# Kernel tuning notes

Hardware: AMD Instinct MI355X
Metric: run time of the kernel (lower is better)

## Reference

```python
import jax, jax.numpy as jnp
import numpy as np

C = 128  # n_atom_basis


def setup_inputs() -> dict:
    key = jax.random.key(0)
    k_h, k_A, k_Ww, k_Wb, k_aw, k_ab = jax.random.split(key, 6)
    B, N = 8, 2048
    h = jax.random.normal(k_h, (B, N, C), dtype=jnp.float32)
    A = jax.random.uniform(k_A, (B, N, N), dtype=jnp.float32)
    # nn.Linear(C, C)
    lim_W = 1.0 / np.sqrt(C)
    W_w = jax.random.uniform(k_Ww, (C, C), minval=-lim_W, maxval=lim_W, dtype=jnp.float32)
    W_b = jax.random.uniform(k_Wb, (C,), minval=-lim_W, maxval=lim_W, dtype=jnp.float32)
    # nn.Linear(2C, 1)
    lim_a = 1.0 / np.sqrt(2 * C)
    a_w = jax.random.uniform(k_aw, (2 * C,), minval=-lim_a, maxval=lim_a, dtype=jnp.float32)
    a_b = jax.random.uniform(k_ab, (), minval=-lim_a, maxval=lim_a, dtype=jnp.float32)
    return {"h": h, "A": A, "W_w": W_w, "W_b": W_b, "a_w": a_w, "a_b": a_b}


def reference(h, A, W_w, W_b, a_w, a_b):
    # Wh computed once ([B,N,C]) instead of the original's redundant [B,N,N,C] broadcast.
    Wh = jnp.einsum('bnc,dc->bnd', h, W_w) + W_b
    # a([hi, hj]) = a_w[:C]@Wh_i + a_w[C:]@Wh_j + a_b  -> rank-1 decomposition of the concat-linear
    si = Wh @ a_w[:C]          # [B,N]
    sj = Wh @ a_w[C:]          # [B,N]
    s = si[:, :, None] + sj[:, None, :] + a_b  # [B,N,N] raw scores
    e = jnp.exp(s) * A                          # masked exp (no max-subtraction: matches original math)
    alpha = e / jnp.sum(e, axis=2, keepdims=True)
    # weighted sum over neighbors j of the ORIGINAL h (as in the source, not Wh)
    h_prime = jnp.einsum('bij,bjc->bic', alpha, h)
    return h_prime
```

## Files before the change

### kernel.cpp

```cpp
#include <hip/hip_runtime.h>
#include <math.h>
#include <stdint.h>

#define Bn 8
#define Nn 2048
#define Cn 128
#define CP 144
#define NKB (Nn / 32)

typedef _Float16 f16x8 __attribute__((ext_vector_type(8)));
typedef _Float16 f16x2 __attribute__((ext_vector_type(2)));
typedef __fp16   fp16x2 __attribute__((ext_vector_type(2)));
typedef float    f32x4 __attribute__((ext_vector_type(4)));

__device__ __forceinline__ void dma16(const void* g, void* l) {
    __builtin_amdgcn_global_load_lds((const __attribute__((address_space(1))) uint32_t*)g,
                                     (__attribute__((address_space(3))) uint32_t*)l,
                                     16, 0, 0);
}

__global__ __launch_bounds__(256) void rows_kernel(const float* __restrict__ h,
                                                   const float* __restrict__ Ww,
                                                   const float* __restrict__ Wb,
                                                   const float* __restrict__ aw,
                                                   _Float16* __restrict__ hWt) {
    __shared__ float tile[16][132];
    __shared__ float vlo[128];
    __shared__ float vhi[128];
    __shared__ float wsh[16];
    __shared__ float b2sh;

    int bid = blockIdx.x;
    int b   = bid & 7;
    int n0  = (bid >> 3) << 4;
    int tid = threadIdx.x;

    {
        int c = tid & 127, half = tid >> 7;
        float acc = 0.f;
#pragma unroll
        for (int dd = 0; dd < 64; ++dd) {
            int d = half * 64 + dd;
            acc += Ww[d * Cn + c] * aw[Cn + d];
        }
        if (half) vhi[c] = acc; else vlo[c] = acc;
    }
    if (tid < 64) {
        float b2p = Wb[tid] * aw[Cn + tid] + Wb[tid + 64] * aw[Cn + tid + 64];
        b2p += __shfl_xor(b2p, 32, 64);
        b2p += __shfl_xor(b2p, 16, 64);
        b2p += __shfl_xor(b2p, 8, 64);
        b2p += __shfl_xor(b2p, 4, 64);
        b2p += __shfl_xor(b2p, 2, 64);
        b2p += __shfl_xor(b2p, 1, 64);
        if (tid == 0) b2sh = b2p;
    }
    {
#pragma unroll
        for (int i = 0; i < 2; ++i) {
            int idx = tid + 256 * i;
            int r = idx >> 5, f4 = idx & 31;
            *(float4*)&tile[r][f4 * 4] =
                ((const float4*)(h + (size_t)(b * Nn + n0 + r) * Cn))[f4];
        }
    }
    __syncthreads();

    {
        int r = tid >> 4, g = tid & 15;
        float acc = 0.f;
#pragma unroll
        for (int ii = 0; ii < 8; ++ii) {
            int i = g * 8 + ii;
            acc += tile[r][i] * (vlo[i] + vhi[i]);
        }
        acc += __shfl_xor(acc, 1, 64);
        acc += __shfl_xor(acc, 2, 64);
        acc += __shfl_xor(acc, 4, 64);
        acc += __shfl_xor(acc, 8, 64);
        if (g == 0) wsh[r] = expf(acc + b2sh);
    }
    __syncthreads();

    {
        int kb = n0 >> 5, khalf = (n0 >> 4) & 1;
        _Float16* hWb = hWt + ((size_t)(b * NKB + kb) * CP) * 32 + khalf * 16;
#pragma unroll
        for (int i = 0; i < 5; ++i) {
            int idx = tid + 256 * i;
            if (idx < 1152) {
                int cp = idx >> 3, p = idx & 7;
                int r0 = p * 2;
                f16x2 v2;
                if (cp < 128) {
                    v2[0] = (_Float16)(wsh[r0] * tile[r0][cp]);
                    v2[1] = (_Float16)(wsh[r0 + 1] * tile[r0 + 1][cp]);
                } else if (cp == 128) {
                    v2[0] = (_Float16)wsh[r0];
                    v2[1] = (_Float16)wsh[r0 + 1];
                } else {
                    v2[0] = (_Float16)0.f;
                    v2[1] = (_Float16)0.f;
                }
                *(f16x2*)(hWb + (size_t)cp * 32 + p * 2) = v2;
            }
        }
    }
}

__global__ __launch_bounds__(256, 4) void attn_kernel(const float* __restrict__ A,
                                                      const _Float16* __restrict__ hWt,
                                                      float* __restrict__ out) {
    __shared__ float Alds[2][16 * 64];
    __shared__ float den[16];

    int bid = blockIdx.x;
    int b   = bid & 7;
    int i0  = (bid >> 3) << 4;
    int koff = ((bid >> 3) * 5 + (bid & 7)) & 31;
    int tid = threadIdx.x;
    int wv  = tid >> 6, l = tid & 63;
    int m   = l & 15, q = l >> 4;

    const float*    Ab  = A   + (size_t)(b * Nn + i0) * Nn;
    const _Float16* hWb = hWt + (size_t)b * NKB * CP * 32;

    int sr  = wv * 4 + q;
    int skq = (m - sr) & 15;
    const float* sg = Ab + (size_t)sr * Nn + skq * 4;
    float* sl = &Alds[0][0] + wv * 256;

    f32x4 acc[3];
#pragma unroll
    for (int s = 0; s < 3; ++s) acc[s] = (f32x4){0.f, 0.f, 0.f, 0.f};

    dma16(sg + (size_t)koff * 64, sl);

    for (int t = 0; t < 32; ++t) {
        int buf = t & 1;
        __syncthreads();
        if (t < 31)
            dma16(sg + (size_t)((t + 1 + koff) & 31) * 64,
                  sl + (buf ^ 1) * (16 * 64));

        int kb = (t + koff) & 31;
        f16x8 bf[6];
#pragma unroll
        for (int ksub = 0; ksub < 2; ++ksub)
#pragma unroll
            for (int s = 0; s < 3; ++s) {
                int ct = (s == 2) ? 8 : wv * 2 + s;
                bf[ksub * 3 + s] = *(const f16x8*)(
                    hWb + ((size_t)(kb * 2 + ksub) * CP + ct * 16 + m) * 32 + q * 8);
            }
#pragma unroll
        for (int ksub = 0; ksub < 2; ++ksub) {
            int kq0 = ksub * 8 + 2 * q;
            float4 x = *(const float4*)&Alds[buf][m * 64 + ((kq0 + m) & 15) * 4];
            float4 y = *(const float4*)&Alds[buf][m * 64 + ((kq0 + 1 + m) & 15) * 4];
            union { fp16x2 h2[4]; f16x8 v; } u;
            u.h2[0] = __builtin_amdgcn_cvt_pkrtz(x.x, x.y);
            u.h2[1] = __builtin_amdgcn_cvt_pkrtz(x.z, x.w);
            u.h2[2] = __builtin_amdgcn_cvt_pkrtz(y.x, y.y);
            u.h2[3] = __builtin_amdgcn_cvt_pkrtz(y.z, y.w);
#pragma unroll
            for (int s = 0; s < 3; ++s)
                acc[s] = __builtin_amdgcn_mfma_f32_16x16x32_f16(u.v, bf[ksub * 3 + s],
                                                                acc[s], 0, 0, 0);
        }
    }

    if (wv == 0 && m == 0) {
#pragma unroll
        for (int r = 0; r < 4; ++r) den[q * 4 + r] = acc[2][r];
    }
    __syncthreads();

#pragma unroll
    for (int r = 0; r < 4; ++r) {
        float invd = 1.f / den[q * 4 + r];
        float* ob = out + (size_t)(b * Nn + i0 + q * 4 + r) * Cn;
#pragma unroll
        for (int s = 0; s < 2; ++s)
            ob[(wv * 2 + s) * 16 + m] = acc[s][r] * invd;
    }
}

extern "C" void kernel_launch(void* const* d_in, const int* in_sizes, int n_in,
                              void* d_out, int out_size, void* d_ws, size_t ws_size,
                              hipStream_t stream) {
    const float* h  = (const float*)d_in[0];
    const float* A  = (const float*)d_in[1];
    const float* Ww = (const float*)d_in[2];
    const float* Wb = (const float*)d_in[3];
    const float* aw = (const float*)d_in[4];
    float* out = (float*)d_out;

    _Float16* hWt = (_Float16*)d_ws;

    rows_kernel<<<Bn * (Nn / 16), 256, 0, stream>>>(h, Ww, Wb, aw, hWt);
    attn_kernel<<<Bn * (Nn / 16), 256, 0, stream>>>(A, hWt, out);
}
```

Baseline: 242.9 us.

## Enlarge attention tile to 32 rows with register-staged fp16 A in LDS

The attention kernel now processes 32 query rows per block with 512 threads. Each wave owns one 16-column output tile across two row tiles, so each hW B-fragment load is reused twice. A is loaded into registers, converted to fp16 once, and stored in LDS. This replaces the async global-to-LDS DMA of fp32 and the per-wave reconversion. The change is meant to halve B-operand traffic per output and cut conversion work, at the cost of a synchronous register-staged prefetch pipeline and the loss of the staggered k-offset.

```diff
diff --git a/kernel.cpp b/kernel.cpp
--- a/kernel.cpp
+++ b/kernel.cpp
@@ -9,15 +9,10 @@
 #define NKB (Nn / 32)
 
 typedef _Float16 f16x8 __attribute__((ext_vector_type(8)));
+typedef _Float16 f16x4 __attribute__((ext_vector_type(4)));
 typedef _Float16 f16x2 __attribute__((ext_vector_type(2)));
 typedef __fp16   fp16x2 __attribute__((ext_vector_type(2)));
 typedef float    f32x4 __attribute__((ext_vector_type(4)));
-
-__device__ __forceinline__ void dma16(const void* g, void* l) {
-    __builtin_amdgcn_global_load_lds((const __attribute__((address_space(1))) uint32_t*)g,
-                                     (__attribute__((address_space(3))) uint32_t*)l,
-                                     16, 0, 0);
-}
 
 __global__ __launch_bounds__(256) void rows_kernel(const float* __restrict__ h,
                                                    const float* __restrict__ Ww,
@@ -108,16 +103,15 @@
     }
 }
 
-__global__ __launch_bounds__(256, 4) void attn_kernel(const float* __restrict__ A,
+__global__ __launch_bounds__(512, 4) void attn_kernel(const float* __restrict__ A,
                                                       const _Float16* __restrict__ hWt,
                                                       float* __restrict__ out) {
-    __shared__ float Alds[2][16 * 64];
-    __shared__ float den[16];
+    __shared__ _Float16 Af[2][2][32][40];
+    __shared__ float den[32];
 
     int bid = blockIdx.x;
     int b   = bid & 7;
-    int i0  = (bid >> 3) << 4;
-    int koff = ((bid >> 3) * 5 + (bid & 7)) & 31;
+    int i0  = (bid >> 3) << 5;
     int tid = threadIdx.x;
     int wv  = tid >> 6, l = tid & 63;
     int m   = l & 15, q = l >> 4;
@@ -125,64 +119,83 @@
     const float*    Ab  = A   + (size_t)(b * Nn + i0) * Nn;
     const _Float16* hWb = hWt + (size_t)b * NKB * CP * 32;
 
-    int sr  = wv * 4 + q;
-    int skq = (m - sr) & 15;
-    const float* sg = Ab + (size_t)sr * Nn + skq * 4;
-    float* sl = &Alds[0][0] + wv * 256;
-
-    f32x4 acc[3];
-#pragma unroll
-    for (int s = 0; s < 3; ++s) acc[s] = (f32x4){0.f, 0.f, 0.f, 0.f};
-
-    dma16(sg + (size_t)koff * 64, sl);
-
-    for (int t = 0; t < 32; ++t) {
-        int buf = t & 1;
+    int sr = tid >> 4, sf4 = tid & 15;
+    const float* sg = Ab + (size_t)sr * Nn + sf4 * 4;
+    int sch = sf4 >> 3, skl = (sf4 & 7) * 4;
+
+    f32x4 accc[2];
+    f32x4 acc8;
+    accc[0] = (f32x4){0.f, 0.f, 0.f, 0.f};
+    accc[1] = (f32x4){0.f, 0.f, 0.f, 0.f};
+    acc8    = (f32x4){0.f, 0.f, 0.f, 0.f};
+
+    auto loadA = [&](int t) { return *(const float4*)(sg + t * 64); };
+    auto storeA = [&](int t, float4 v) {
+        union { fp16x2 h2[2]; f16x4 v4; } u;
+        u.h2[0] = __builtin_amdgcn_cvt_pkrtz(v.x, v.y);
+        u.h2[1] = __builtin_amdgcn_cvt_pkrtz(v.z, v.w);
+        *(f16x4*)&Af[t & 1][sch][sr][skl] = u.v4;
+    };
+    auto loadB = [&](int t, f16x8* bf) {
+#pragma unroll
+        for (int ck = 0; ck < 2; ++ck)
+            bf[ck] = *(const f16x8*)(hWb + ((size_t)(2 * t + ck) * CP + wv * 16 + m) * 32 + q * 8);
+        if (wv < 2) {
+#pragma unroll
+            for (int ck = 0; ck < 2; ++ck)
+                bf[2 + ck] = *(const f16x8*)(hWb + ((size_t)(2 * t + ck) * CP + 128 + m) * 32 + q * 8);
+        }
+    };
+    auto compute = [&](int buf, const f16x8* bf) {
+#pragma unroll
+        for (int ck = 0; ck < 2; ++ck) {
+            f16x8 af0 = *(const f16x8*)&Af[buf][ck][m][q * 8];
+            f16x8 af1 = *(const f16x8*)&Af[buf][ck][16 + m][q * 8];
+            accc[0] = __builtin_amdgcn_mfma_f32_16x16x32_f16(af0, bf[ck], accc[0], 0, 0, 0);
+            accc[1] = __builtin_amdgcn_mfma_f32_16x16x32_f16(af1, bf[ck], accc[1], 0, 0, 0);
+            if (wv < 2)
+                acc8 = __builtin_amdgcn_mfma_f32_16x16x32_f16(wv ? af1 : af0, bf[2 + ck],
+                                                              acc8, 0, 0, 0);
+        }
+    };
+
+    float4 a0 = loadA(0);
+    float4 a1 = loadA(1);
+    f16x8 bfA[4], bfB[4];
+    loadB(0, bfA);
+    storeA(0, a0);
+    __syncthreads();
+
+    for (int t2 = 0; t2 < 16; ++t2) {
+        int te = 2 * t2, to = te + 1;
+        loadB(to, bfB);
+        if (t2 < 15) a0 = loadA(te + 2);
+        compute(0, bfA);
+        storeA(to, a1);
         __syncthreads();
-        if (t < 31)
-            dma16(sg + (size_t)((t + 1 + koff) & 31) * 64,
-                  sl + (buf ^ 1) * (16 * 64));
-
-        int kb = (t + koff) & 31;
-        f16x8 bf[6];
-#pragma unroll
-        for (int ksub = 0; ksub < 2; ++ksub)
-#pragma unroll
-            for (int s = 0; s < 3; ++s) {
-                int ct = (s == 2) ? 8 : wv * 2 + s;
-                bf[ksub * 3 + s] = *(const f16x8*)(
-                    hWb + ((size_t)(kb * 2 + ksub) * CP + ct * 16 + m) * 32 + q * 8);
-            }
-#pragma unroll
-        for (int ksub = 0; ksub < 2; ++ksub) {
-            int kq0 = ksub * 8 + 2 * q;
-            float4 x = *(const float4*)&Alds[buf][m * 64 + ((kq0 + m) & 15) * 4];
-            float4 y = *(const float4*)&Alds[buf][m * 64 + ((kq0 + 1 + m) & 15) * 4];
-            union { fp16x2 h2[4]; f16x8 v; } u;
-            u.h2[0] = __builtin_amdgcn_cvt_pkrtz(x.x, x.y);
-            u.h2[1] = __builtin_amdgcn_cvt_pkrtz(x.z, x.w);
-            u.h2[2] = __builtin_amdgcn_cvt_pkrtz(y.x, y.y);
-            u.h2[3] = __builtin_amdgcn_cvt_pkrtz(y.z, y.w);
-#pragma unroll
-            for (int s = 0; s < 3; ++s)
-                acc[s] = __builtin_amdgcn_mfma_f32_16x16x32_f16(u.v, bf[ksub * 3 + s],
-                                                                acc[s], 0, 0, 0);
-        }
-    }
-
-    if (wv == 0 && m == 0) {
-#pragma unroll
-        for (int r = 0; r < 4; ++r) den[q * 4 + r] = acc[2][r];
-    }
-    __syncthreads();
-
-#pragma unroll
-    for (int r = 0; r < 4; ++r) {
-        float invd = 1.f / den[q * 4 + r];
-        float* ob = out + (size_t)(b * Nn + i0 + q * 4 + r) * Cn;
-#pragma unroll
-        for (int s = 0; s < 2; ++s)
-            ob[(wv * 2 + s) * 16 + m] = acc[s][r] * invd;
+        if (t2 < 15) {
+            loadB(to + 1, bfA);
+            a1 = loadA(to + 2);
+        }
+        compute(1, bfB);
+        if (t2 < 15) storeA(to + 1, a0);
+        __syncthreads();
+    }
+
+    if (wv < 2 && m == 0) {
+#pragma unroll
+        for (int r = 0; r < 4; ++r) den[wv * 16 + q * 4 + r] = acc8[r];
+    }
+    __syncthreads();
+
+#pragma unroll
+    for (int mt = 0; mt < 2; ++mt) {
+#pragma unroll
+        for (int r = 0; r < 4; ++r) {
+            int row = mt * 16 + q * 4 + r;
+            float invd = 1.f / den[row];
+            out[(size_t)(b * Nn + i0 + row) * Cn + wv * 16 + m] = accc[mt][r] * invd;
+        }
     }
 }
 
@@ -199,5 +212,5 @@
     _Float16* hWt = (_Float16*)d_ws;
 
     rows_kernel<<<Bn * (Nn / 16), 256, 0, stream>>>(h, Ww, Wb, aw, hWt);
-    attn_kernel<<<Bn * (Nn / 16), 256, 0, stream>>>(A, hWt, out);
+    attn_kernel<<<Bn * (Nn / 32), 512, 0, stream>>>(A, hWt, out);
 }
```

New measurement: 226.0 us. 1.07x faster.
